# Performance work log

Measured on AMD Instinct MI355X. Metric: run time of the kernel, lower is better.

## Reference

```python
import jax, jax.numpy as jnp
import numpy as np

GROUP_SIZE = 128
IN_FEATURES = 4096
OUT_FEATURES = 11008
BATCH = 16


def setup_inputs() -> dict:
    key = jax.random.key(0)
    k_x, k_q, k_s, k_z, k_b = jax.random.split(key, 5)
    num_groups = IN_FEATURES // GROUP_SIZE
    x = jax.random.normal(k_x, (BATCH, IN_FEATURES), dtype=jnp.float32)
    # packed int4 pairs stored as bytes in [0, 256)
    qweight = jax.random.randint(k_q, (OUT_FEATURES, IN_FEATURES // 2), 0, 256, dtype=jnp.int32)
    # positive scales of realistic magnitude, zeros in [0, 15]
    scales = jax.random.uniform(k_s, (OUT_FEATURES, num_groups), dtype=jnp.float32) * 0.01 + 1e-4
    zeros = jax.random.uniform(k_z, (OUT_FEATURES, num_groups), dtype=jnp.float32) * 15.0
    bias = jax.random.normal(k_b, (OUT_FEATURES,), dtype=jnp.float32)
    return {"x": x, "qweight": qweight, "scales": scales, "zeros": zeros, "bias": bias}


def _unpack_int4(packed, in_features):
    # packed: [O, I//2] ints in [0,256); low nibble is even column, high nibble odd
    low = packed & 15
    high = (packed >> 4) & 15
    return jnp.stack([low, high], axis=-1).reshape(packed.shape[0], in_features)  # [O, I]


def reference(x, qweight, scales, zeros, bias):
    q = _unpack_int4(qweight, IN_FEATURES).astype(jnp.float32)        # [O, I]
    s = jnp.repeat(scales, GROUP_SIZE, axis=1)                        # [O, I]
    z = jnp.repeat(zeros, GROUP_SIZE, axis=1)                         # [O, I]
    w = (q - z) * s                                                   # dequantized weight [O, I]
    return x @ w.T + bias                                             # [B, O]
```

## Files before the change

kernel.cpp:

```cpp
#include <hip/hip_runtime.h>
#include <hip/hip_fp16.h>

#define IN_F   4096
#define OUT_F  11008
#define BATCH  16
#define GROUPS 32
#define PACKED_PER_ROW (IN_F / 2)

typedef __attribute__((ext_vector_type(8))) _Float16 half8;
typedef __attribute__((ext_vector_type(4))) _Float16 half4;
typedef __attribute__((ext_vector_type(2))) _Float16 h2;
typedef __attribute__((ext_vector_type(4))) float    float4_t;
typedef __attribute__((ext_vector_type(4))) int      int4_t;
typedef __attribute__((ext_vector_type(4))) unsigned uint4_t;

__device__ inline h2 cvt2(float a, float b) {
    return __builtin_bit_cast(h2, __builtin_amdgcn_cvt_pkrtz(a, b));
}

__global__ __launch_bounds__(256) void xcvt(const float* __restrict__ x,
                                            _Float16* __restrict__ xh) {
    const int i = (blockIdx.x * 256 + threadIdx.x) * 4;
    const float4_t v = *(const float4_t*)(x + i);
    half4 h;
    h2 lo = cvt2(v.x, v.y), hi = cvt2(v.z, v.w);
    h[0] = lo[0]; h[1] = lo[1]; h[2] = hi[0]; h[3] = hi[1];
    *(half4*)(xh + i) = h;
}

__global__ __launch_bounds__(64) void gptq_gemm_w(
    const _Float16* __restrict__ xh, const int* __restrict__ qw,
    const float* __restrict__ scales, const float* __restrict__ zeros,
    float* __restrict__ ws_part)
{
    const int lane  = threadIdx.x;
    const int otile = blockIdx.x >> 2;
    const int kq    = blockIdx.x & 3;

    const int ln = lane & 15;
    const int lk = lane >> 4;
    const int o  = otile * 16 + ln;

    const int*      qaddr = qw + o * PACKED_PER_ROW + kq * 512 + lk * 4;
    const _Float16* xaddr = xh + ln * IN_F + kq * 1024 + lk * 8;

    const float4_t sf0 = *(const float4_t*)(scales + o * GROUPS + kq * 8);
    const float4_t sf1 = *(const float4_t*)(scales + o * GROUPS + kq * 8 + 4);
    const float4_t zf0 = *(const float4_t*)(zeros  + o * GROUPS + kq * 8);
    const float4_t zf1 = *(const float4_t*)(zeros  + o * GROUPS + kq * 8 + 4);
    const float sArr[8] = { sf0.x, sf0.y, sf0.z, sf0.w, sf1.x, sf1.y, sf1.z, sf1.w };
    const float zArr[8] = { zf0.x, zf0.y, zf0.z, zf0.w, zf1.x, zf1.y, zf1.z, zf1.w };
    h2 s2g[8], c2g[8];
    #pragma unroll
    for (int gi = 0; gi < 8; ++gi) {
        const float s  = sArr[gi];
        const float c0 = -zArr[gi] * s;
        s2g[gi] = cvt2(s, s);
        c2g[gi] = cvt2(c0, c0);
    }

    int4_t qv[2][8];
    half8  xv[2][8];
    const h2 k1024 = { (_Float16)1024.0f, (_Float16)1024.0f };

#define GLQ(B,T,OFF) asm volatile("global_load_dwordx4 %0, %1, off offset:%2" \
                                  : "=v"(qv[B][T]) : "v"(qaddr), "n"(OFF));
#define GLX(B,T,OFF) asm volatile("global_load_dwordx4 %0, %1, off offset:%2" \
                                  : "=v"(xv[B][T]) : "v"(xaddr), "n"(OFF));
#define LOAD_CHUNK(B, CB) \
    GLQ(B,0,CB+0)   GLX(B,0,CB+0)   GLQ(B,1,CB+64)  GLX(B,1,CB+64)  \
    GLQ(B,2,CB+128) GLX(B,2,CB+128) GLQ(B,3,CB+192) GLX(B,3,CB+192) \
    GLQ(B,4,CB+256) GLX(B,4,CB+256) GLQ(B,5,CB+320) GLX(B,5,CB+320) \
    GLQ(B,6,CB+384) GLX(B,6,CB+384) GLQ(B,7,CB+448) GLX(B,7,CB+448)

#define VWAIT16 { asm volatile("s_waitcnt vmcnt(16)" ::: "memory"); \
                  __builtin_amdgcn_sched_barrier(0); }
#define VWAIT0  { asm volatile("s_waitcnt vmcnt(0)"  ::: "memory"); \
                  __builtin_amdgcn_sched_barrier(0); }

#define COMPUTE(B, C) { \
    _Pragma("unroll") \
    for (int t = 0; t < 8; ++t) { \
        const int gi = 2*(C) + (t >> 2); \
        uint4_t bw; \
        _Pragma("unroll") \
        for (int i = 0; i < 4; ++i) { \
            const unsigned pv = (unsigned)qv[B][t][i]; \
            const unsigned u = (pv & 0xFu) | ((pv << 12) & 0xF0000u) \
                             | 0x64006400u;              \
            h2 q = __builtin_bit_cast(h2, u) - k1024;    \
            h2 w = q * s2g[gi] + c2g[gi];                \
            bw[i] = __builtin_bit_cast(unsigned, w); \
        } \
        acc = __builtin_amdgcn_mfma_f32_16x16x32_f16( \
            xv[B][t], __builtin_bit_cast(half8, bw), acc, 0, 0, 0); \
    } }

    float4_t acc = {0.f, 0.f, 0.f, 0.f};

    LOAD_CHUNK(0, 0)
    LOAD_CHUNK(1, 512)

    VWAIT16
    COMPUTE(0, 0)
    LOAD_CHUNK(0, 1024)

    VWAIT16
    COMPUTE(1, 1)
    LOAD_CHUNK(1, 1536)

    VWAIT16
    COMPUTE(0, 2)

    VWAIT0
    COMPUTE(1, 3)

    #pragma unroll
    for (int r = 0; r < 4; ++r)
        ws_part[(kq * BATCH + lk * 4 + r) * OUT_F + otile * 16 + ln] = acc[r];

#undef GLQ
#undef GLX
#undef LOAD_CHUNK
#undef VWAIT16
#undef VWAIT0
#undef COMPUTE
}

__global__ __launch_bounds__(256) void gptq_reduce(
    const float* __restrict__ ws_part, const float* __restrict__ bias,
    float* __restrict__ out)
{
    const int idx = blockIdx.x * 256 + threadIdx.x;
    if (idx >= BATCH * OUT_F) return;
    const int o = idx % OUT_F;
    out[idx] = bias[o]
             + ws_part[idx]
             + ws_part[1 * (BATCH * OUT_F) + idx]
             + ws_part[2 * (BATCH * OUT_F) + idx]
             + ws_part[3 * (BATCH * OUT_F) + idx];
}

__global__ __launch_bounds__(256) void gptq_gemm_fb(
    const float* __restrict__ x, const int* __restrict__ qw,
    const float* __restrict__ scales, const float* __restrict__ zeros,
    const float* __restrict__ bias, float* __restrict__ out)
{
    const int tid  = threadIdx.x;
    const int lane = tid & 63;
    const int wave = tid >> 6;
    const int otile = blockIdx.x;
    const int ln = lane & 15, lk = lane >> 4;
    const int o = otile * 16 + ln;
    const int kc0 = wave * 1024;

    const int* qbase = qw + o * PACKED_PER_ROW + (kc0 >> 1) + lk * 4;
    const float* srow = scales + o * GROUPS;
    const float* zrow = zeros  + o * GROUPS;

    float4_t acc = {0.f, 0.f, 0.f, 0.f};
    const h2 k1024 = { (_Float16)1024.0f, (_Float16)1024.0f };

    #pragma unroll
    for (int ch = 0; ch < 4; ++ch) {
        const int cc = kc0 + ch * 256;
        h2 s2[2], c2[2];
        #pragma unroll
        for (int gi = 0; gi < 2; ++gi) {
            const float s  = srow[(cc >> 7) + gi];
            const float c0 = -zrow[(cc >> 7) + gi] * s;
            s2[gi] = cvt2(s, s); c2[gi] = cvt2(c0, c0);
        }
        #pragma unroll
        for (int t = 0; t < 8; ++t) {
            const int4_t v = *(const int4_t*)(qbase + ch * 128 + t * 16);
            const float* xp = x + ln * IN_F + cc + t * 32 + lk * 8;
            const float4_t a0 = *(const float4_t*)(xp);
            const float4_t a1 = *(const float4_t*)(xp + 4);
            half8 af;
            h2 p0 = cvt2(a0.x, a0.y), p1 = cvt2(a0.z, a0.w);
            h2 p2 = cvt2(a1.x, a1.y), p3 = cvt2(a1.z, a1.w);
            af[0]=p0[0]; af[1]=p0[1]; af[2]=p1[0]; af[3]=p1[1];
            af[4]=p2[0]; af[5]=p2[1]; af[6]=p3[0]; af[7]=p3[1];
            const int gi = t >> 2;
            uint4_t bw;
            #pragma unroll
            for (int i = 0; i < 4; ++i) {
                const unsigned pv = (unsigned)v[i];
                const unsigned u = (pv & 0xFu) | ((pv << 12) & 0xF0000u)
                                 | 0x64006400u;
                h2 q = __builtin_bit_cast(h2, u) - k1024;
                h2 w = q * s2[gi] + c2[gi];
                bw[i] = __builtin_bit_cast(unsigned, w);
            }
            acc = __builtin_amdgcn_mfma_f32_16x16x32_f16(
                af, __builtin_bit_cast(half8, bw), acc, 0, 0, 0);
        }
    }

    __shared__ float red[4][16][17];
    #pragma unroll
    for (int r = 0; r < 4; ++r) red[wave][lk * 4 + r][ln] = acc[r];
    __syncthreads();
    const int row = tid >> 4, col = tid & 15;
    const float sum = red[0][row][col] + red[1][row][col]
                    + red[2][row][col] + red[3][row][col];
    const int oo = otile * 16 + col;
    out[row * OUT_F + oo] = sum + bias[oo];
}

extern "C" void kernel_launch(void* const* d_in, const int* in_sizes, int n_in,
                              void* d_out, int out_size, void* d_ws, size_t ws_size,
                              hipStream_t stream) {
    const float* x      = (const float*)d_in[0];
    const int*   qwgt   = (const int*)d_in[1];
    const float* scales = (const float*)d_in[2];
    const float* zeros  = (const float*)d_in[3];
    const float* bias   = (const float*)d_in[4];
    float* out = (float*)d_out;

    const int nOTiles = OUT_F / 16;
    const size_t need = (size_t)8 << 20;

    if (d_ws && ws_size >= need) {
        float*    ws_part = (float*)d_ws;
        _Float16* xh      = (_Float16*)((char*)d_ws + (4 << 20));
        hipLaunchKernelGGL(xcvt, dim3(BATCH * IN_F / 1024), dim3(256), 0, stream,
                           x, xh);
        hipLaunchKernelGGL(gptq_gemm_w, dim3(nOTiles * 4), dim3(64), 0, stream,
                           xh, qwgt, scales, zeros, ws_part);
        hipLaunchKernelGGL(gptq_reduce, dim3((BATCH * OUT_F + 255) / 256),
                           dim3(256), 0, stream, ws_part, bias, out);
    } else {
        hipLaunchKernelGGL(gptq_gemm_fb, dim3(nOTiles), dim3(256), 0, stream,
                           x, qwgt, scales, zeros, bias, out);
    }
}
```

Baseline: 35.19 us.

## Stage packed weights through LDS with direct global-to-LDS loads and 4-wave blocks

Restructures the main GEMM kernel from single-wave blocks that load weights and activations into registers into 256-thread blocks. These blocks stream packed int4 weights straight into shared memory with global_load_lds, using an XOR swizzle to avoid bank conflicts, in two halves. Activations are pre-converted to fp16 in an MFMA-fragment-permuted layout so each lane does one contiguous 16-byte load. Each wave handles one K-chunk and the four waves are reduced through shared memory. The aim is better load coalescing and fewer registers, at the cost of extra barriers and an LDS reduction, with less explicit software prefetching than before.

```diff
diff --git a/kernel.cpp b/kernel.cpp
--- a/kernel.cpp
+++ b/kernel.cpp
@@ -5,10 +5,9 @@
 #define OUT_F  11008
 #define BATCH  16
 #define GROUPS 32
-#define PACKED_PER_ROW (IN_F / 2)
+#define PPR    2048
 
 typedef __attribute__((ext_vector_type(8))) _Float16 half8;
-typedef __attribute__((ext_vector_type(4))) _Float16 half4;
 typedef __attribute__((ext_vector_type(2))) _Float16 h2;
 typedef __attribute__((ext_vector_type(4))) float    float4_t;
 typedef __attribute__((ext_vector_type(4))) int      int4_t;
@@ -18,112 +17,105 @@
     return __builtin_bit_cast(h2, __builtin_amdgcn_cvt_pkrtz(a, b));
 }
 
-__global__ __launch_bounds__(256) void xcvt(const float* __restrict__ x,
-                                            _Float16* __restrict__ xh) {
-    const int i = (blockIdx.x * 256 + threadIdx.x) * 4;
-    const float4_t v = *(const float4_t*)(x + i);
-    half4 h;
-    h2 lo = cvt2(v.x, v.y), hi = cvt2(v.z, v.w);
-    h[0] = lo[0]; h[1] = lo[1]; h[2] = hi[0]; h[3] = hi[1];
-    *(half4*)(xh + i) = h;
-}
-
-__global__ __launch_bounds__(64) void gptq_gemm_w(
-    const _Float16* __restrict__ xh, const int* __restrict__ qw,
+#define GLOAD_LDS(srcp, ldsp) \
+    __builtin_amdgcn_global_load_lds( \
+        (const __attribute__((address_space(1))) void*)(srcp), \
+        (__attribute__((address_space(3))) void*)(ldsp), 16, 0, 0)
+
+__global__ __launch_bounds__(256) void xcvt_perm(const float* __restrict__ x,
+                                                 _Float16* __restrict__ xp) {
+    const int T = blockIdx.x * 256 + threadIdx.x;
+    const int step = T >> 6, lane = T & 63;
+    const int b = lane & 15, k = step * 32 + (lane >> 4) * 8;
+    const float4_t a0 = *(const float4_t*)(x + b * IN_F + k);
+    const float4_t a1 = *(const float4_t*)(x + b * IN_F + k + 4);
+    half8 h;
+    h2 p0 = cvt2(a0.x, a0.y), p1 = cvt2(a0.z, a0.w);
+    h2 p2 = cvt2(a1.x, a1.y), p3 = cvt2(a1.z, a1.w);
+    h[0]=p0[0]; h[1]=p0[1]; h[2]=p1[0]; h[3]=p1[1];
+    h[4]=p2[0]; h[5]=p2[1]; h[6]=p3[0]; h[7]=p3[1];
+    *(half8*)(xp + step * 512 + lane * 8) = h;
+}
+
+__global__ __launch_bounds__(256) void gptq_gemm_w(
+    const _Float16* __restrict__ xp, const int* __restrict__ qw,
     const float* __restrict__ scales, const float* __restrict__ zeros,
     float* __restrict__ ws_part)
 {
-    const int lane  = threadIdx.x;
-    const int otile = blockIdx.x >> 2;
-    const int kq    = blockIdx.x & 3;
-
-    const int ln = lane & 15;
-    const int lk = lane >> 4;
+    __shared__ int   lq[16 * 512];
+    __shared__ float red[4][16][17];
+
+    const int tid  = threadIdx.x;
+    const int lane = tid & 63, wave = tid >> 6;
+    const int otile = blockIdx.x >> 2, kq = blockIdx.x & 3;
+    const int ln = lane & 15, lk = lane >> 4;
     const int o  = otile * 16 + ln;
 
-    const int*      qaddr = qw + o * PACKED_PER_ROW + kq * 512 + lk * 4;
-    const _Float16* xaddr = xh + ln * IN_F + kq * 1024 + lk * 8;
-
-    const float4_t sf0 = *(const float4_t*)(scales + o * GROUPS + kq * 8);
-    const float4_t sf1 = *(const float4_t*)(scales + o * GROUPS + kq * 8 + 4);
-    const float4_t zf0 = *(const float4_t*)(zeros  + o * GROUPS + kq * 8);
-    const float4_t zf1 = *(const float4_t*)(zeros  + o * GROUPS + kq * 8 + 4);
-    const float sArr[8] = { sf0.x, sf0.y, sf0.z, sf0.w, sf1.x, sf1.y, sf1.z, sf1.w };
-    const float zArr[8] = { zf0.x, zf0.y, zf0.z, zf0.w, zf1.x, zf1.y, zf1.z, zf1.w };
-    h2 s2g[8], c2g[8];
-    #pragma unroll
-    for (int gi = 0; gi < 8; ++gi) {
-        const float s  = sArr[gi];
-        const float c0 = -zArr[gi] * s;
-        s2g[gi] = cvt2(s, s);
-        c2g[gi] = cvt2(c0, c0);
-    }
-
-    int4_t qv[2][8];
-    half8  xv[2][8];
+    #pragma unroll
+    for (int i = 0; i < 4; ++i) {
+        const int row = wave * 4 + i;
+        const int* src = qw + (otile * 16 + row) * PPR + kq * 512
+                       + ((lane ^ (row & 7)) * 4);
+        GLOAD_LDS(src, &lq[row * 512]);
+    }
+
+    const int c = wave;
+    const int g = kq * 8 + c * 2;
+    const float s0 = scales[o * GROUPS + g], s1 = scales[o * GROUPS + g + 1];
+    const float z0 = zeros [o * GROUPS + g], z1 = zeros [o * GROUPS + g + 1];
+    const h2 s2[2] = { cvt2(s0, s0), cvt2(s1, s1) };
+    const h2 c2[2] = { cvt2(-z0 * s0, -z0 * s0), cvt2(-z1 * s1, -z1 * s1) };
     const h2 k1024 = { (_Float16)1024.0f, (_Float16)1024.0f };
-
-#define GLQ(B,T,OFF) asm volatile("global_load_dwordx4 %0, %1, off offset:%2" \
-                                  : "=v"(qv[B][T]) : "v"(qaddr), "n"(OFF));
-#define GLX(B,T,OFF) asm volatile("global_load_dwordx4 %0, %1, off offset:%2" \
-                                  : "=v"(xv[B][T]) : "v"(xaddr), "n"(OFF));
-#define LOAD_CHUNK(B, CB) \
-    GLQ(B,0,CB+0)   GLX(B,0,CB+0)   GLQ(B,1,CB+64)  GLX(B,1,CB+64)  \
-    GLQ(B,2,CB+128) GLX(B,2,CB+128) GLQ(B,3,CB+192) GLX(B,3,CB+192) \
-    GLQ(B,4,CB+256) GLX(B,4,CB+256) GLQ(B,5,CB+320) GLX(B,5,CB+320) \
-    GLQ(B,6,CB+384) GLX(B,6,CB+384) GLQ(B,7,CB+448) GLX(B,7,CB+448)
-
-#define VWAIT16 { asm volatile("s_waitcnt vmcnt(16)" ::: "memory"); \
-                  __builtin_amdgcn_sched_barrier(0); }
-#define VWAIT0  { asm volatile("s_waitcnt vmcnt(0)"  ::: "memory"); \
-                  __builtin_amdgcn_sched_barrier(0); }
-
-#define COMPUTE(B, C) { \
+    const int x3 = ln & 7;
+
+    float4_t acc = {0.f, 0.f, 0.f, 0.f};
+
+#define COMPUTE(C) { \
     _Pragma("unroll") \
     for (int t = 0; t < 8; ++t) { \
-        const int gi = 2*(C) + (t >> 2); \
+        const int4_t v = *(const int4_t*)((const char*)lq + ln * 2048 \
+                        + (((C) * 32 + ((t * 4 + lk) ^ x3)) << 4)); \
+        const half8 af = *(const half8*)(xp + (kq * 32 + (C) * 8 + t) * 512 \
+                        + lane * 8); \
+        const int gi = t >> 2; \
         uint4_t bw; \
         _Pragma("unroll") \
         for (int i = 0; i < 4; ++i) { \
-            const unsigned pv = (unsigned)qv[B][t][i]; \
+            const unsigned pv = (unsigned)v[i]; \
             const unsigned u = (pv & 0xFu) | ((pv << 12) & 0xF0000u) \
-                             | 0x64006400u;              \
-            h2 q = __builtin_bit_cast(h2, u) - k1024;    \
-            h2 w = q * s2g[gi] + c2g[gi];                \
+                             | 0x64006400u;             \
+            h2 q = __builtin_bit_cast(h2, u) - k1024;   \
+            h2 w = q * s2[gi] + c2[gi];                 \
             bw[i] = __builtin_bit_cast(unsigned, w); \
         } \
         acc = __builtin_amdgcn_mfma_f32_16x16x32_f16( \
-            xv[B][t], __builtin_bit_cast(half8, bw), acc, 0, 0, 0); \
+            af, __builtin_bit_cast(half8, bw), acc, 0, 0, 0); \
     } }
 
-    float4_t acc = {0.f, 0.f, 0.f, 0.f};
-
-    LOAD_CHUNK(0, 0)
-    LOAD_CHUNK(1, 512)
-
-    VWAIT16
-    COMPUTE(0, 0)
-    LOAD_CHUNK(0, 1024)
-
-    VWAIT16
-    COMPUTE(1, 1)
-    LOAD_CHUNK(1, 1536)
-
-    VWAIT16
-    COMPUTE(0, 2)
-
-    VWAIT0
-    COMPUTE(1, 3)
-
-    #pragma unroll
-    for (int r = 0; r < 4; ++r)
-        ws_part[(kq * BATCH + lk * 4 + r) * OUT_F + otile * 16 + ln] = acc[r];
-
-#undef GLQ
-#undef GLX
-#undef LOAD_CHUNK
-#undef VWAIT16
-#undef VWAIT0
+    __syncthreads();
+
+    #pragma unroll
+    for (int i = 0; i < 4; ++i) {
+        const int row = wave * 4 + i;
+        const int* src = qw + (otile * 16 + row) * PPR + kq * 512 + 256
+                       + ((lane ^ (row & 7)) * 4);
+        GLOAD_LDS(src, &lq[row * 512 + 256]);
+    }
+
+    if (wave < 2) COMPUTE(c)
+
+    __syncthreads();
+
+    if (wave >= 2) COMPUTE(c)
+
+    #pragma unroll
+    for (int r = 0; r < 4; ++r) red[wave][lk * 4 + r][ln] = acc[r];
+    __syncthreads();
+
+    const int row = tid >> 4, col = tid & 15;
+    const float sum = red[0][row][col] + red[1][row][col]
+                    + red[2][row][col] + red[3][row][col];
+    ws_part[(kq * BATCH + row) * OUT_F + otile * 16 + col] = sum;
 #undef COMPUTE
 }
 
@@ -154,7 +146,7 @@
     const int o = otile * 16 + ln;
     const int kc0 = wave * 1024;
 
-    const int* qbase = qw + o * PACKED_PER_ROW + (kc0 >> 1) + lk * 4;
+    const int* qbase = qw + o * PPR + (kc0 >> 1) + lk * 4;
     const float* srow = scales + o * GROUPS;
     const float* zrow = zeros  + o * GROUPS;
 
@@ -174,9 +166,9 @@
         #pragma unroll
         for (int t = 0; t < 8; ++t) {
             const int4_t v = *(const int4_t*)(qbase + ch * 128 + t * 16);
-            const float* xp = x + ln * IN_F + cc + t * 32 + lk * 8;
-            const float4_t a0 = *(const float4_t*)(xp);
-            const float4_t a1 = *(const float4_t*)(xp + 4);
+            const float* xq = x + ln * IN_F + cc + t * 32 + lk * 8;
+            const float4_t a0 = *(const float4_t*)(xq);
+            const float4_t a1 = *(const float4_t*)(xq + 4);
             half8 af;
             h2 p0 = cvt2(a0.x, a0.y), p1 = cvt2(a0.z, a0.w);
             h2 p2 = cvt2(a1.x, a1.y), p3 = cvt2(a1.z, a1.w);
@@ -224,11 +216,10 @@
 
     if (d_ws && ws_size >= need) {
         float*    ws_part = (float*)d_ws;
-        _Float16* xh      = (_Float16*)((char*)d_ws + (4 << 20));
-        hipLaunchKernelGGL(xcvt, dim3(BATCH * IN_F / 1024), dim3(256), 0, stream,
-                           x, xh);
-        hipLaunchKernelGGL(gptq_gemm_w, dim3(nOTiles * 4), dim3(64), 0, stream,
-                           xh, qwgt, scales, zeros, ws_part);
+        _Float16* xp      = (_Float16*)((char*)d_ws + (4 << 20));
+        hipLaunchKernelGGL(xcvt_perm, dim3(32), dim3(256), 0, stream, x, xp);
+        hipLaunchKernelGGL(gptq_gemm_w, dim3(nOTiles * 4), dim3(256), 0, stream,
+                           xp, qwgt, scales, zeros, ws_part);
         hipLaunchKernelGGL(gptq_reduce, dim3((BATCH * OUT_F + 255) / 256),
                            dim3(256), 0, stream, ws_part, bias, out);
     } else {
```

Result: faster. 30.61 us (-13.0%).
